# Performance work log

Measured on AMD Instinct MI355X. Metric: run time of the kernel, lower is better.

## Reference

```python
import jax, jax.numpy as jnp
import numpy as np

N = 40000      # nodes
E = 640000     # edges
D = 128        # embed_dim
H = 8          # heads
DH = D // H    # per-head dim
L = 3          # n_layers
IN = 64        # in_dim
FF = 218       # embed_dim2 (ffn hidden)
OUT = 1        # out_dim
EPS = 1e-5
NEG_SLOPE = 0.2


def setup_inputs() -> dict:
    key = jax.random.key(0)
    ks = jax.random.split(key, 16)
    nrm = lambda k, shape, s=0.1: (jax.random.normal(k, shape, jnp.float32) * s)
    return {
        "x": jax.random.normal(ks[0], (N, IN), jnp.float32),
        "src": jax.random.randint(ks[1], (E,), 0, N, jnp.int32),
        "dst": jax.random.randint(ks[2], (E,), 0, N, jnp.int32),
        "W_emb": nrm(ks[3], (IN, D)),
        "b_emb": jnp.zeros((D,), jnp.float32),
        "gat_W": nrm(ks[4], (L, D, D)),
        "attn_l": nrm(ks[5], (L, H, DH)),
        "attn_r": nrm(ks[6], (L, H, DH)),
        "gat_b": jnp.zeros((L, D), jnp.float32),
        "bn1_g": jnp.ones((L, D), jnp.float32),
        "bn1_b": jnp.zeros((L, D), jnp.float32),
        "ff_W1": nrm(ks[7], (L, D, FF)),
        "ff_b1": jnp.zeros((L, FF), jnp.float32),
        "ff_W2": nrm(ks[8], (L, FF, D)),
        "ff_b2": jnp.zeros((L, D), jnp.float32),
        "bn2_g": jnp.ones((L, D), jnp.float32),
        "bn2_b": jnp.zeros((L, D), jnp.float32),
        "dec_W1": nrm(ks[9], ((L + 1) * D, D)),
        "dec_bn_g": jnp.ones((D,), jnp.float32),
        "dec_bn_b": jnp.zeros((D,), jnp.float32),
        "dec_W2": nrm(ks[10], (D, OUT)),
    }


def _batchnorm(h, g, b):
    # BatchNorm1d in training mode: batch stats over nodes, biased variance
    mu = h.mean(axis=0)
    var = h.var(axis=0)
    return g * (h - mu) * jax.lax.rsqrt(var + EPS) + b


def _gat_layer(h, src, dst, W, al, ar, bias):
    n = h.shape[0]
    feat = (h @ W).reshape(n, H, DH)                      # [N,H,DH]
    el = (feat * al).sum(-1)                               # [N,H]
    er = (feat * ar).sum(-1)                               # [N,H]
    e = jax.nn.leaky_relu(el[src] + er[dst], NEG_SLOPE)    # [E,H]
    # segment softmax over incoming edges of each dst node
    emax = jax.ops.segment_max(e, dst, num_segments=n)
    ex = jnp.exp(e - emax[dst])
    den = jax.ops.segment_sum(ex, dst, num_segments=n)
    alpha = ex / den[dst]                                  # [E,H]
    msg = alpha[:, :, None] * feat[src]                    # [E,H,DH]
    out = jax.ops.segment_sum(msg, dst, num_segments=n)    # [N,H,DH]
    out = out + bias.reshape(H, DH)
    return out.reshape(n, D)


def reference(x, src, dst, W_emb, b_emb, gat_W, attn_l, attn_r, gat_b,
              bn1_g, bn1_b, ff_W1, ff_b1, ff_W2, ff_b2, bn2_g, bn2_b,
              dec_W1, dec_bn_g, dec_bn_b, dec_W2):
    h = x @ W_emb + b_emb                                  # embed_layer
    xs = [h]
    for l in range(L):
        # message passing with skip connection
        h = h + _gat_layer(h, src, dst, gat_W[l], attn_l[l], attn_r[l], gat_b[l])
        # feed forward: BN -> Skip(Linear,ReLU,Linear) -> BN
        h = _batchnorm(h, bn1_g[l], bn1_b[l])
        y = jax.nn.relu(h @ ff_W1[l] + ff_b1[l]) @ ff_W2[l] + ff_b2[l]
        h = _batchnorm(h + y, bn2_g[l], bn2_b[l])
        xs.append(h)
    h = jnp.concatenate(xs, axis=-1)                       # JumpingKnowledge 'cat'
    # decision MLP: relu(BN(h W1)) W2, no biases
    h = jax.nn.relu(_batchnorm(h @ dec_W1, dec_bn_g, dec_bn_b))
    return h @ dec_W2
```

## Files before the change

### kernel.cpp

```cpp
#include <hip/hip_runtime.h>
#include <hip/hip_bf16.h>
#include <math.h>

#define N_NODES 40000
#define N_EDGES 640000
#define DIM     128
#define HEADS   8
#define DHEAD   16
#define LAYERS  3
#define IN_DIM  64
#define FF_DIM  218
#define BN_EPS  1e-5f
#define NEG_SLOPE 0.2f
#define INV_N   (1.f / N_NODES)
#define NREP    128
#define AGG_NPW 2
#define AGG_BLOCKS (N_NODES / (4 * AGG_NPW))

typedef __attribute__((ext_vector_type(8))) short  bhalf8;
typedef __attribute__((ext_vector_type(4))) float  floatx4;
typedef __attribute__((ext_vector_type(4))) int    intx4;

__device__ __forceinline__ unsigned bfpack2(float a, float b) {
    unsigned ua = __float_as_uint(a);
    ua = ua + 0x7FFFu + ((ua >> 16) & 1u);
    unsigned ub = __float_as_uint(b);
    ub = ub + 0x7FFFu + ((ub >> 16) & 1u);
    return (ua >> 16) | (ub & 0xFFFF0000u);
}
__device__ __forceinline__ unsigned short bf16of(float a) {
    unsigned ua = __float_as_uint(a);
    ua = ua + 0x7FFFu + ((ua >> 16) & 1u);
    return (unsigned short)(ua >> 16);
}
__device__ __forceinline__ float bf2f(unsigned short u) {
    return __uint_as_float(((unsigned)u) << 16);
}
__device__ __forceinline__ float bflo(unsigned u) { return __uint_as_float(u << 16); }
__device__ __forceinline__ float bfhi(unsigned u) { return __uint_as_float(u & 0xFFFF0000u); }
__device__ __forceinline__ float rsum16(float v) {
    v += __shfl_xor(v, 1, 16);
    v += __shfl_xor(v, 2, 16);
    v += __shfl_xor(v, 4, 16);
    v += __shfl_xor(v, 8, 16);
    return v;
}

#define OFF_EMB 0
#define OFF_GAT 8192
#define OFF_W1  57344
#define OFF_W2  143360
#define OFF_DEC 229376
#define WPK_TOT 294912
#define HIST_BLOCKS ((N_EDGES + 255) / 256)
#define PACK_BLOCKS ((WPK_TOT + 255) / 256)

__global__ void hist_pack_kernel(const int* __restrict__ dst, int* __restrict__ counts,
                                 const float* __restrict__ W_emb,
                                 const float* __restrict__ gat_W,
                                 const float* __restrict__ ff_W1,
                                 const float* __restrict__ ff_W2,
                                 const float* __restrict__ dec_W1,
                                 unsigned short* __restrict__ wpk) {
    int bid = blockIdx.x;
    if (bid < HIST_BLOCKS) {
        int e = bid * 256 + threadIdx.x;
        if (e < N_EDGES) atomicAdd(&counts[dst[e]], 1);
        return;
    }
    int i = (bid - HIST_BLOCKS) * 256 + threadIdx.x;
    if (i >= WPK_TOT) return;
    int o = i;
    if (o < 8192) {
        int n = o >> 6, k = o & 63;
        wpk[OFF_EMB + o] = bf16of(W_emb[k * 128 + n]);
        return;
    }
    o -= 8192;
    if (o < 3 * 16384) {
        int l = o >> 14, r = o & 16383;
        int n = r >> 7, k = r & 127;
        wpk[OFF_GAT + o] = bf16of(gat_W[l * 16384 + k * 128 + n]);
        return;
    }
    o -= 3 * 16384;
    if (o < 3 * 28672) {
        int l = o / 28672, r = o % 28672;
        int n = r >> 7, k = r & 127;
        float v = (n < FF_DIM) ? ff_W1[(size_t)l * 128 * FF_DIM + k * FF_DIM + n] : 0.f;
        wpk[OFF_W1 + o] = bf16of(v);
        return;
    }
    o -= 3 * 28672;
    if (o < 3 * 28672) {
        int l = o / 28672, r = o % 28672;
        int n = r / 224, k = r % 224;
        float v = (k < FF_DIM) ? ff_W2[(size_t)l * FF_DIM * 128 + k * 128 + n] : 0.f;
        wpk[OFF_W2 + o] = bf16of(v);
        return;
    }
    o -= 3 * 28672;
    {
        int n = o >> 9, k = o & 511;
        wpk[OFF_DEC + o] = bf16of(dec_W1[k * 128 + n]);
    }
}

__global__ __launch_bounds__(1024) void scan_kernel(const int* __restrict__ counts,
                                                    int* __restrict__ indptr,
                                                    int* __restrict__ cursor, int n) {
    __shared__ int tsum[1024];
    const int CH = 40;
    int tid = threadIdx.x;
    int base = tid * CH;
    int loc[CH];
    int s = 0;
    #pragma unroll
    for (int i = 0; i < CH; i++) {
        int idx = base + i;
        int v = (idx < n) ? counts[idx] : 0;
        loc[i] = s;
        s += v;
    }
    tsum[tid] = s;
    __syncthreads();
    for (int offs = 1; offs < 1024; offs <<= 1) {
        int t = (tid >= offs) ? tsum[tid - offs] : 0;
        __syncthreads();
        tsum[tid] += t;
        __syncthreads();
    }
    int carry = (tid > 0) ? tsum[tid - 1] : 0;
    #pragma unroll
    for (int i = 0; i < CH; i++) {
        int idx = base + i;
        if (idx < n) {
            int v = carry + loc[i];
            indptr[idx] = v;
            cursor[idx] = v;
        }
    }
    if (tid == 1023) indptr[n] = tsum[1023];
}

__global__ void scatter_kernel(const int* __restrict__ src, const int* __restrict__ dst,
                               int* __restrict__ cursor,
                               int* __restrict__ srcs_csr) {
    int e = blockIdx.x * blockDim.x + threadIdx.x;
    if (e < N_EDGES) {
        int d = dst[e];
        int pos = atomicAdd(&cursor[d], 1);
        srcs_csr[pos] = src[e];
    }
}

template<int NT, int KPAD, int AMODE, bool ABF16, int MT, bool ELER, bool RESBF>
__global__ __launch_bounds__(256) void gemm_l2_kernel(
    const float* __restrict__ A, const unsigned short* __restrict__ Abf, int lda,
    const unsigned short* __restrict__ Bpk,
    const float* __restrict__ bias,
    const void* __restrict__ resv, int ldres,
    const float* __restrict__ res_stats, const float* __restrict__ res_g,
    const float* __restrict__ res_b,
    float* __restrict__ C, unsigned short* __restrict__ Cbf, int ldc,
    float* __restrict__ out_stats,
    int M, int Nact, int relu,
    const float* __restrict__ a_stats, float* __restrict__ a_stats_out,
    const float* __restrict__ a_g, const float* __restrict__ a_b,
    const float* __restrict__ al, const float* __restrict__ ar,
    float* __restrict__ el_out, float* __restrict__ er_out)
{
    constexpr int SCN = (AMODE > 0) ? KPAD : 1;
    constexpr int BROWS = 64 * MT;
    constexpr int STEPS = KPAD / 32;
    constexpr int CST = (STEPS > 2) ? 2 : STEPS;
    __shared__ float sc_s[SCN];
    __shared__ float sh_s[SCN];
    __shared__ float st_sum[128];
    __shared__ float st_sq[128];
    __shared__ float el_s[ELER ? BROWS : 1][ELER ? NT : 1];
    __shared__ float er_s[ELER ? BROWS : 1][ELER ? NT : 1];

    int tid = threadIdx.x, wave = tid >> 6, lane = tid & 63;
    int q = lane >> 4, tl = lane & 15;
    int colbase = blockIdx.y * (NT * 16);
    int row0b = blockIdx.x * BROWS;
    int rowtile = row0b + wave * (MT * 16);

    if constexpr (AMODE == 1 || AMODE == 2) {
        for (int idx = tid; idx < KPAD; idx += 256) {
            float scv = 1.f, shv = 0.f;
            if constexpr (AMODE == 1) {
                float mu = a_stats[idx] * INV_N;
                float var = a_stats[128 + idx] * INV_N - mu * mu;
                scv = a_g[idx] * rsqrtf(var + BN_EPS);
                shv = a_b[idx] - mu * scv;
            } else {
                int l = idx >> 7;
                if (l > 0) {
                    int c = idx & 127;
                    const float* st = a_stats + (l - 1) * 256;
                    float mu = st[c] * INV_N;
                    float var = st[128 + c] * INV_N - mu * mu;
                    scv = a_g[(l - 1) * 128 + c] * rsqrtf(var + BN_EPS);
                    shv = a_b[(l - 1) * 128 + c] - mu * scv;
                }
            }
            sc_s[idx] = scv;
            sh_s[idx] = shv;
        }
        __syncthreads();
    }
    if constexpr (AMODE == 3) {
        for (int idx = tid; idx < 128; idx += 256) {
            float s = 0.f, sq = 0.f;
            #pragma unroll 8
            for (int r = 0; r < NREP; r++) {
                s  += a_stats[r * 256 + idx];
                sq += a_stats[r * 256 + 128 + idx];
            }
            a_stats_out[idx] = s;
            a_stats_out[128 + idx] = sq;
            float mu = s * INV_N;
            float var = sq * INV_N - mu * mu;
            float scv = a_g[idx] * rsqrtf(var + BN_EPS);
            sc_s[idx] = scv;
            sh_s[idx] = a_b[idx] - mu * scv;
        }
        __syncthreads();
    }

    int rowm[MT];
    bool vrm[MT];
    #pragma unroll
    for (int mt = 0; mt < MT; mt++) {
        rowm[mt] = rowtile + mt * 16 + tl;
        vrm[mt] = rowm[mt] < M;
    }
    const unsigned short* bp = Bpk + (size_t)colbase * KPAD;

    floatx4 acc[MT][NT] = {};

    #pragma unroll
    for (int c0 = 0; c0 < STEPS; c0 += CST) {
        intx4  arawb[CST][MT];
        floatx4 araw0[ABF16 ? 1 : CST][ABF16 ? 1 : MT];
        floatx4 araw1[ABF16 ? 1 : CST][ABF16 ? 1 : MT];
        bhalf8 breg[CST][NT];
        #pragma unroll
        for (int cs = 0; cs < CST; cs++) {
            if (c0 + cs >= STEPS) continue;
            int gk = (c0 + cs) * 32 + q * 8;
            #pragma unroll
            for (int j = 0; j < NT; j++)
                breg[cs][j] = *(const bhalf8*)(bp + (size_t)(j * 16 + tl) * KPAD + gk);
            #pragma unroll
            for (int mt = 0; mt < MT; mt++) {
                if constexpr (ABF16) {
                    intx4 u = {};
                    if (vrm[mt]) u = *(const intx4*)(Abf + (size_t)rowm[mt] * lda + gk);
                    arawb[cs][mt] = u;
                } else {
                    floatx4 x0 = {}, x1 = {};
                    if (vrm[mt]) {
                        const float* ap = A + (size_t)rowm[mt] * lda + gk;
                        x0 = *(const floatx4*)ap;
                        x1 = *(const floatx4*)(ap + 4);
                    }
                    araw0[cs][mt] = x0;
                    araw1[cs][mt] = x1;
                }
            }
        }
        #pragma unroll
        for (int cs = 0; cs < CST; cs++) {
            if (c0 + cs >= STEPS) continue;
            int gk = (c0 + cs) * 32 + q * 8;
            bhalf8 af[MT];
            #pragma unroll
            for (int mt = 0; mt < MT; mt++) {
                if constexpr (ABF16) {
                    intx4 u = arawb[cs][mt];
                    if constexpr (AMODE > 0) {
                        #pragma unroll
                        for (int w = 0; w < 4; w++) {
                            unsigned uw = (unsigned)u[w];
                            float lo = bflo(uw), hi = bfhi(uw);
                            lo = fmaf(sc_s[gk + 2 * w],     lo, sh_s[gk + 2 * w]);
                            hi = fmaf(sc_s[gk + 2 * w + 1], hi, sh_s[gk + 2 * w + 1]);
                            u[w] = (int)bfpack2(lo, hi);
                        }
                    }
                    af[mt] = *(bhalf8*)&u;
                } else {
                    floatx4 x0 = araw0[cs][mt], x1 = araw1[cs][mt];
                    if constexpr (AMODE > 0) {
                        #pragma unroll
                        for (int jj = 0; jj < 4; jj++) {
                            x0[jj] = fmaf(sc_s[gk + jj],     x0[jj], sh_s[gk + jj]);
                            x1[jj] = fmaf(sc_s[gk + 4 + jj], x1[jj], sh_s[gk + 4 + jj]);
                        }
                    }
                    intx4 t = intx4{(int)bfpack2(x0[0], x0[1]), (int)bfpack2(x0[2], x0[3]),
                                    (int)bfpack2(x1[0], x1[1]), (int)bfpack2(x1[2], x1[3])};
                    af[mt] = *(bhalf8*)&t;
                }
            }
            #pragma unroll
            for (int mt = 0; mt < MT; mt++)
                #pragma unroll
                for (int j = 0; j < NT; j++)
                    acc[mt][j] = __builtin_amdgcn_mfma_f32_16x16x32_bf16(af[mt], breg[cs][j], acc[mt][j], 0, 0, 0);
        }
    }

    float psum[NT], psq[NT];
    #pragma unroll
    for (int j = 0; j < NT; j++) { psum[j] = 0.f; psq[j] = 0.f; }

    #pragma unroll
    for (int j = 0; j < NT; j++) {
        int c = colbase + j * 16 + tl;
        bool cok = c < Nact;
        float bv = (bias && cok) ? bias[c] : 0.f;
        float rsc = 1.f, rsh = 0.f;
        if (res_stats && cok) {
            float mu = res_stats[c] * INV_N;
            float var = res_stats[128 + c] * INV_N - mu * mu;
            rsc = res_g[c] * rsqrtf(var + BN_EPS);
            rsh = res_b[c] - mu * rsc;
        }
        float alc = 0.f, arc = 0.f;
        if constexpr (ELER) { alc = al[c]; arc = ar[c]; }
        #pragma unroll
        for (int mt = 0; mt < MT; mt++) {
            #pragma unroll
            for (int reg = 0; reg < 4; reg++) {
                int r = rowtile + mt * 16 + q * 4 + reg;
                bool rok = r < M;
                float v = 0.f;
                if (rok && cok) {
                    v = acc[mt][j][reg] + bv;
                    if (resv) {
                        size_t ri = (size_t)r * ldres + c;
                        float rv = RESBF ? bf2f(((const unsigned short*)resv)[ri])
                                         : ((const float*)resv)[ri];
                        v = fmaf(rsc, rv, v + rsh);
                    }
                    if (relu) v = fmaxf(v, 0.f);
                    if (out_stats) { psum[j] += v; psq[j] = fmaf(v, v, psq[j]); }
                }
                if constexpr (ELER) {
                    float pel = rsum16(v * alc);
                    float per_ = rsum16(v * arc);
                    if (tl == 0) {
                        int rl = wave * (MT * 16) + mt * 16 + q * 4 + reg;
                        el_s[rl][j] = pel;
                        er_s[rl][j] = per_;
                    }
                }
                if (rok) {
                    if (Cbf) Cbf[(size_t)r * ldc + c] = bf16of(v);
                    else if (cok) C[(size_t)r * ldc + c] = v;
                }
            }
        }
    }

    if constexpr (ELER) {
        __syncthreads();
        int gh = blockIdx.y * NT;
        for (int idx = tid; idx < BROWS * NT; idx += 256) {
            int rl = idx / NT, hj = idx % NT;
            int r = row0b + rl;
            if (r < M) {
                el_out[(size_t)r * 8 + gh + hj] = el_s[rl][hj];
                er_out[(size_t)r * 8 + gh + hj] = er_s[rl][hj];
            }
        }
    }

    if (out_stats) {
        __syncthreads();
        if (tid < 128) { st_sum[tid] = 0.f; st_sq[tid] = 0.f; }
        __syncthreads();
        #pragma unroll
        for (int j = 0; j < NT; j++) {
            int c = colbase + j * 16 + tl;
            if (c < 128) { atomicAdd(&st_sum[c], psum[j]); atomicAdd(&st_sq[c], psq[j]); }
        }
        __syncthreads();
        if (tid < 128) {
            atomicAdd(&out_stats[tid], st_sum[tid]);
            atomicAdd(&out_stats[128 + tid], st_sq[tid]);
        }
    }
}

__global__ __launch_bounds__(256) void gat_aggregate_kernel(
    const unsigned short* __restrict__ feat,
    const float* __restrict__ el, const float* __restrict__ er,
    const int* __restrict__ indptr, const int* __restrict__ srcs_csr,
    const unsigned short* __restrict__ h_in, int ldh,
    const float* __restrict__ hstats, const float* __restrict__ hg,
    const float* __restrict__ hb,
    const float* __restrict__ bias,
    unsigned short* __restrict__ outp,
    float* __restrict__ stats_rep)
{
    int t = threadIdx.x;
    int w = t >> 6, lane = t & 63;
    int d0 = lane * 2;
    int hh = lane >> 3;
    int pick = lane & 3;
    int gb = lane & 56;
    __shared__ float sred[4][128];
    __shared__ float qred[4][128];

    float aff_s0 = 1.f, aff_h0 = 0.f, aff_s1 = 1.f, aff_h1 = 0.f;
    if (hstats) {
        float mu0 = hstats[d0] * INV_N;
        float v0  = hstats[128 + d0] * INV_N - mu0 * mu0;
        aff_s0 = hg[d0] * rsqrtf(v0 + BN_EPS);
        aff_h0 = hb[d0] - mu0 * aff_s0;
        float mu1 = hstats[d0 + 1] * INV_N;
        float v1  = hstats[128 + d0 + 1] * INV_N - mu1 * mu1;
        aff_s1 = hg[d0 + 1] * rsqrtf(v1 + BN_EPS);
        aff_h1 = hb[d0 + 1] - mu1 * aff_s1;
    }
    float b0 = bias[d0], b1 = bias[d0 + 1];

    float ss0 = 0.f, sq0 = 0.f, ss1 = 0.f, sq1 = 0.f;
    int nbase = (blockIdx.x * 4 + w) * AGG_NPW;
    #pragma unroll
    for (int ni = 0; ni < AGG_NPW; ni++) {
        int n = nbase + ni;
        if (n >= N_NODES) break;
        int beg = indptr[n], end = indptr[n + 1];
        float ern = er[(size_t)n * 8 + hh];
        float acc0 = 0.f, acc1 = 0.f, den = 0.f;
        int i = beg;
        for (; i + 3 < end; i += 4) {
            int s0 = srcs_csr[i],     s1 = srcs_csr[i + 1];
            int s2 = srcs_csr[i + 2], s3 = srcs_csr[i + 3];
            int sp = pick == 0 ? s0 : pick == 1 ? s1 : pick == 2 ? s2 : s3;
            float ee = el[(size_t)sp * 8 + hh] + ern;
            unsigned f0 = *(const unsigned*)(feat + (size_t)s0 * DIM + d0);
            unsigned f1 = *(const unsigned*)(feat + (size_t)s1 * DIM + d0);
            unsigned f2 = *(const unsigned*)(feat + (size_t)s2 * DIM + d0);
            unsigned f3 = *(const unsigned*)(feat + (size_t)s3 * DIM + d0);
            float aa = expf(ee > 0.f ? ee : NEG_SLOPE * ee);
            float a0 = __shfl(aa, gb + 0);
            float a1 = __shfl(aa, gb + 1);
            float a2 = __shfl(aa, gb + 2);
            float a3 = __shfl(aa, gb + 3);
            den += (a0 + a1) + (a2 + a3);
            acc0 = fmaf(a0, bflo(f0), acc0); acc1 = fmaf(a0, bfhi(f0), acc1);
            acc0 = fmaf(a1, bflo(f1), acc0); acc1 = fmaf(a1, bfhi(f1), acc1);
            acc0 = fmaf(a2, bflo(f2), acc0); acc1 = fmaf(a2, bfhi(f2), acc1);
            acc0 = fmaf(a3, bflo(f3), acc0); acc1 = fmaf(a3, bfhi(f3), acc1);
        }
        for (; i < end; i++) {
            int s0 = srcs_csr[i];
            float e0 = el[(size_t)s0 * 8 + hh] + ern;
            unsigned f0 = *(const unsigned*)(feat + (size_t)s0 * DIM + d0);
            float a0 = expf(e0 > 0.f ? e0 : NEG_SLOPE * e0);
            den += a0;
            acc0 = fmaf(a0, bflo(f0), acc0);
            acc1 = fmaf(a0, bfhi(f0), acc1);
        }
        float inv = den > 0.f ? 1.f / den : 0.f;
        unsigned hu = *(const unsigned*)(h_in + (size_t)n * ldh + d0);
        float hv0 = fmaf(aff_s0, bflo(hu), aff_h0);
        float hv1 = fmaf(aff_s1, bfhi(hu), aff_h1);
        unsigned short u0 = bf16of(hv0 + acc0 * inv + b0);
        unsigned short u1 = bf16of(hv1 + acc1 * inv + b1);
        *(unsigned*)(outp + (size_t)n * DIM + d0) = ((unsigned)u0) | (((unsigned)u1) << 16);
        float vr0 = bf2f(u0), vr1 = bf2f(u1);
        ss0 += vr0; sq0 = fmaf(vr0, vr0, sq0);
        ss1 += vr1; sq1 = fmaf(vr1, vr1, sq1);
    }
    sred[w][d0] = ss0; sred[w][d0 + 1] = ss1;
    qred[w][d0] = sq0; qred[w][d0 + 1] = sq1;
    __syncthreads();
    {
        int d = t & 127;
        float v = (t < 128)
            ? (sred[0][d] + sred[1][d]) + (sred[2][d] + sred[3][d])
            : (qred[0][d] + qred[1][d]) + (qred[2][d] + qred[3][d]);
        float* rep = stats_rep + ((size_t)(blockIdx.x & (NREP - 1)) << 8);
        atomicAdd(&rep[t], v);
    }
}

__global__ __launch_bounds__(256) void decide_kernel(
    const unsigned short* __restrict__ z, const float* __restrict__ stats,
    const float* __restrict__ g, const float* __restrict__ b,
    const float* __restrict__ W2, float* __restrict__ outp, int M)
{
    int wid = threadIdx.x >> 6, lane = threadIdx.x & 63;
    int n = blockIdx.x * 4 + wid;
    if (n >= M) return;
    float acc = 0.f;
    #pragma unroll
    for (int cc = 0; cc < 2; cc++) {
        int c = lane + cc * 64;
        float mu  = stats[c] * INV_N;
        float var = stats[DIM + c] * INV_N - mu * mu;
        float v = fmaf(g[c] * rsqrtf(var + BN_EPS), bf2f(z[(size_t)n * DIM + c]) - mu, b[c]);
        v = fmaxf(v, 0.f);
        acc = fmaf(v, W2[c], acc);
    }
    #pragma unroll
    for (int offs = 32; offs > 0; offs >>= 1)
        acc += __shfl_down(acc, offs);
    if (lane == 0) outp[n] = acc;
}

extern "C" void kernel_launch(void* const* d_in, const int* in_sizes, int n_in,
                              void* d_out, int out_size, void* d_ws, size_t ws_size,
                              hipStream_t stream)
{
    const float* x      = (const float*)d_in[0];
    const int*   src    = (const int*)  d_in[1];
    const int*   dst    = (const int*)  d_in[2];
    const float* W_emb  = (const float*)d_in[3];
    const float* b_emb  = (const float*)d_in[4];
    const float* gat_W  = (const float*)d_in[5];
    const float* attn_l = (const float*)d_in[6];
    const float* attn_r = (const float*)d_in[7];
    const float* gat_b  = (const float*)d_in[8];
    const float* bn1_g  = (const float*)d_in[9];
    const float* bn1_b  = (const float*)d_in[10];
    const float* ff_W1  = (const float*)d_in[11];
    const float* ff_b1  = (const float*)d_in[12];
    const float* ff_W2  = (const float*)d_in[13];
    const float* ff_b2  = (const float*)d_in[14];
    const float* bn2_g  = (const float*)d_in[15];
    const float* bn2_b  = (const float*)d_in[16];
    const float* dec_W1 = (const float*)d_in[17];
    const float* dec_bn_g = (const float*)d_in[18];
    const float* dec_bn_b = (const float*)d_in[19];
    const float* dec_W2 = (const float*)d_in[20];
    float* outp = (float*)d_out;

    char* ws = (char*)d_ws;
    size_t off = 0;
    auto alloc = [&](size_t bytes) -> void* {
        void* p = ws + off;
        off += (bytes + 255) & ~(size_t)255;
        return p;
    };
    unsigned short* xsb = (unsigned short*)alloc((size_t)N_NODES * 512 * 2);
    unsigned short* zb  = (unsigned short*)alloc((size_t)N_NODES * DIM * 2);
    unsigned short* featb = (unsigned short*)alloc((size_t)N_NODES * DIM * 2);
    float* el    = (float*)alloc((size_t)N_NODES * HEADS * 4);
    float* er    = (float*)alloc((size_t)N_NODES * HEADS * 4);
    unsigned short* y1b = (unsigned short*)alloc((size_t)N_NODES * 224 * 2);
    unsigned short* btb = (unsigned short*)alloc((size_t)N_NODES * DIM * 2);
    int*   counts= (int*)  alloc((size_t)N_NODES * 4);
    float* statsAll = (float*)alloc(((size_t)3 * NREP * 256 + 7 * 256) * 4);
    unsigned short* wpk = (unsigned short*)alloc((size_t)WPK_TOT * 2);
    int*   indptr= (int*)  alloc((size_t)(N_NODES + 1) * 4);
    int*   cursor= (int*)  alloc((size_t)N_NODES * 4);
    int*   srcs_csr = (int*)alloc((size_t)N_EDGES * 4);
    (void)ws_size; (void)in_sizes; (void)n_in; (void)out_size;

    float* rep1   = statsAll;
    float* stats1c= statsAll + 3 * NREP * 256;
    float* stats2 = statsAll + 3 * NREP * 256 + 3 * 256;
    float* statsD = statsAll + 3 * NREP * 256 + 6 * 256;

    dim3 gg2((N_NODES + 127) / 128, 2);
    dim3 ggdec((N_NODES + 63) / 64, 2);

    hipMemsetAsync(counts, 0, (size_t)N_NODES * 4 + ((size_t)3 * NREP * 256 + 7 * 256) * 4, stream);
    hist_pack_kernel<<<HIST_BLOCKS + PACK_BLOCKS, 256, 0, stream>>>(
        dst, counts, W_emb, gat_W, ff_W1, ff_W2, dec_W1, wpk);
    scan_kernel<<<1, 1024, 0, stream>>>(counts, indptr, cursor, N_NODES);
    scatter_kernel<<<(N_EDGES + 255) / 256, 256, 0, stream>>>(src, dst, cursor, srcs_csr);

    gemm_l2_kernel<4, 64, 0, false, 2, false, false><<<gg2, 256, 0, stream>>>(
        x, nullptr, IN_DIM, wpk + OFF_EMB, b_emb,
        nullptr, 0, nullptr, nullptr, nullptr,
        nullptr, xsb, 512, nullptr,
        N_NODES, DIM, 0, nullptr, nullptr, nullptr, nullptr,
        nullptr, nullptr, nullptr, nullptr);

    for (int l = 0; l < LAYERS; l++) {
        const unsigned short* h_cur = xsb + (size_t)l * DIM;
        const float* hstats = l ? stats2 + (l - 1) * 256 : nullptr;
        const float* hg = l ? bn2_g + (l - 1) * DIM : nullptr;
        const float* hb = l ? bn2_b + (l - 1) * DIM : nullptr;
        if (l == 0)
            gemm_l2_kernel<4, 128, 0, true, 2, true, false><<<gg2, 256, 0, stream>>>(
                nullptr, h_cur, 512, wpk + OFF_GAT + l * 16384, nullptr,
                nullptr, 0, nullptr, nullptr, nullptr,
                nullptr, featb, DIM, nullptr,
                N_NODES, DIM, 0, nullptr, nullptr, nullptr, nullptr,
                attn_l + l * DIM, attn_r + l * DIM, el, er);
        else
            gemm_l2_kernel<4, 128, 1, true, 2, true, false><<<gg2, 256, 0, stream>>>(
                nullptr, h_cur, 512, wpk + OFF_GAT + l * 16384, nullptr,
                nullptr, 0, nullptr, nullptr, nullptr,
                nullptr, featb, DIM, nullptr,
                N_NODES, DIM, 0, hstats, nullptr, hg, hb,
                attn_l + l * DIM, attn_r + l * DIM, el, er);
        gat_aggregate_kernel<<<AGG_BLOCKS, 256, 0, stream>>>(
            featb, el, er, indptr, srcs_csr, h_cur, 512,
            hstats, hg, hb, gat_b + l * DIM, btb,
            rep1 + (size_t)l * NREP * 256);
        gemm_l2_kernel<7, 128, 3, true, 2, false, false><<<gg2, 256, 0, stream>>>(
            nullptr, btb, DIM, wpk + OFF_W1 + l * 28672,
            ff_b1 + l * FF_DIM,
            nullptr, 0, nullptr, nullptr, nullptr,
            nullptr, y1b, 224, nullptr,
            N_NODES, FF_DIM, 1,
            rep1 + (size_t)l * NREP * 256, stats1c + l * 256,
            bn1_g + l * DIM, bn1_b + l * DIM,
            nullptr, nullptr, nullptr, nullptr);
        gemm_l2_kernel<4, 224, 0, true, 2, false, true><<<gg2, 256, 0, stream>>>(
            nullptr, y1b, 224, wpk + OFF_W2 + l * 28672,
            ff_b2 + l * DIM,
            btb, DIM, stats1c + l * 256, bn1_g + l * DIM, bn1_b + l * DIM,
            nullptr, xsb + (size_t)(l + 1) * DIM, 512, stats2 + l * 256,
            N_NODES, DIM, 0, nullptr, nullptr, nullptr, nullptr,
            nullptr, nullptr, nullptr, nullptr);
    }

    gemm_l2_kernel<4, 512, 2, true, 1, false, false><<<ggdec, 256, 0, stream>>>(
        nullptr, xsb, 512, wpk + OFF_DEC, nullptr,
        nullptr, 0, nullptr, nullptr, nullptr,
        nullptr, zb, DIM, statsD,
        N_NODES, DIM, 0, stats2, nullptr, bn2_g, bn2_b,
        nullptr, nullptr, nullptr, nullptr);
    decide_kernel<<<(N_NODES + 3) / 4, 256, 0, stream>>>(
        zb, statsD, dec_bn_g, dec_bn_b, dec_W2, outp, N_NODES);
}
```

Measured before the change: 716.3 us.

## Stage A tiles in swizzled shared memory for bf16 GEMM kernels

Adds a STAGEA template path where each block cooperatively loads a chunk of up to 128 K-columns of the bf16 A rows into LDS with an XOR swizzle, then waves read their A fragments from LDS. Global A loads become coalesced row-contiguous 16-byte accesses instead of per-lane strided fragment gathers. In exchange it adds shared memory use (up to 32 KB per block at MT=2), __syncthreads barriers, and loses the previous register prefetch overlap of A and B loads. All bf16-input GEMMs switch to this path; the fp32 embedding GEMM keeps the old one.

```diff
diff --git a/kernel.cpp b/kernel.cpp
--- a/kernel.cpp
+++ b/kernel.cpp
@@ -154,7 +154,7 @@
     }
 }
 
-template<int NT, int KPAD, int AMODE, bool ABF16, int MT, bool ELER, bool RESBF>
+template<int NT, int KPAD, int AMODE, bool ABF16, int MT, bool ELER, bool RESBF, bool STAGEA>
 __global__ __launch_bounds__(256) void gemm_l2_kernel(
     const float* __restrict__ A, const unsigned short* __restrict__ Abf, int lda,
     const unsigned short* __restrict__ Bpk,
@@ -180,6 +180,7 @@
     __shared__ float st_sq[128];
     __shared__ float el_s[ELER ? BROWS : 1][ELER ? NT : 1];
     __shared__ float er_s[ELER ? BROWS : 1][ELER ? NT : 1];
+    __shared__ unsigned short As[STAGEA ? BROWS * 128 : 1];
 
     int tid = threadIdx.x, wave = tid >> 6, lane = tid & 63;
     int q = lane >> 4, tl = lane & 15;
@@ -230,57 +231,37 @@
         __syncthreads();
     }
 
-    int rowm[MT];
-    bool vrm[MT];
-    #pragma unroll
-    for (int mt = 0; mt < MT; mt++) {
-        rowm[mt] = rowtile + mt * 16 + tl;
-        vrm[mt] = rowm[mt] < M;
-    }
     const unsigned short* bp = Bpk + (size_t)colbase * KPAD;
 
     floatx4 acc[MT][NT] = {};
 
-    #pragma unroll
-    for (int c0 = 0; c0 < STEPS; c0 += CST) {
-        intx4  arawb[CST][MT];
-        floatx4 araw0[ABF16 ? 1 : CST][ABF16 ? 1 : MT];
-        floatx4 araw1[ABF16 ? 1 : CST][ABF16 ? 1 : MT];
-        bhalf8 breg[CST][NT];
+    if constexpr (STAGEA) {
+        char* asb = (char*)As;
         #pragma unroll
-        for (int cs = 0; cs < CST; cs++) {
-            if (c0 + cs >= STEPS) continue;
-            int gk = (c0 + cs) * 32 + q * 8;
+        for (int ck = 0; ck < STEPS; ck += 4) {
+            int csteps = (STEPS - ck) < 4 ? (STEPS - ck) : 4;
+            int ck16 = csteps * 4;
+            for (int idx = tid; idx < BROWS * ck16; idx += 256) {
+                int lr = idx / ck16, kc = idx - lr * ck16;
+                int rg = row0b + lr;
+                intx4 u = {};
+                if (rg < M) u = *(const intx4*)(Abf + (size_t)rg * lda + ck * 32 + kc * 8);
+                *(intx4*)(asb + lr * 256 + ((kc ^ (lr & 7)) << 4)) = u;
+            }
+            __syncthreads();
             #pragma unroll
-            for (int j = 0; j < NT; j++)
-                breg[cs][j] = *(const bhalf8*)(bp + (size_t)(j * 16 + tl) * KPAD + gk);
-            #pragma unroll
-            for (int mt = 0; mt < MT; mt++) {
-                if constexpr (ABF16) {
-                    intx4 u = {};
-                    if (vrm[mt]) u = *(const intx4*)(Abf + (size_t)rowm[mt] * lda + gk);
-                    arawb[cs][mt] = u;
-                } else {
-                    floatx4 x0 = {}, x1 = {};
-                    if (vrm[mt]) {
-                        const float* ap = A + (size_t)rowm[mt] * lda + gk;
-                        x0 = *(const floatx4*)ap;
-                        x1 = *(const floatx4*)(ap + 4);
-                    }
-                    araw0[cs][mt] = x0;
-                    araw1[cs][mt] = x1;
-                }
-            }
-        }
-        #pragma unroll
-        for (int cs = 0; cs < CST; cs++) {
-            if (c0 + cs >= STEPS) continue;
-            int gk = (c0 + cs) * 32 + q * 8;
-            bhalf8 af[MT];
-            #pragma unroll
-            for (int mt = 0; mt < MT; mt++) {
-                if constexpr (ABF16) {
-                    intx4 u = arawb[cs][mt];
+            for (int cs = 0; cs < 4; cs++) {
+                if (cs >= csteps) break;
+                int gk = (ck + cs) * 32 + q * 8;
+                bhalf8 breg2[NT];
+                #pragma unroll
+                for (int j = 0; j < NT; j++)
+                    breg2[j] = *(const bhalf8*)(bp + (size_t)(j * 16 + tl) * KPAD + gk);
+                bhalf8 af[MT];
+                #pragma unroll
+                for (int mt = 0; mt < MT; mt++) {
+                    int lr = wave * (MT * 16) + mt * 16 + tl;
+                    intx4 u = *(const intx4*)(asb + lr * 256 + (((cs * 4 + q) ^ (lr & 7)) << 4));
                     if constexpr (AMODE > 0) {
                         #pragma unroll
                         for (int w = 0; w < 4; w++) {
@@ -292,25 +273,94 @@
                         }
                     }
                     af[mt] = *(bhalf8*)&u;
-                } else {
-                    floatx4 x0 = araw0[cs][mt], x1 = araw1[cs][mt];
-                    if constexpr (AMODE > 0) {
-                        #pragma unroll
-                        for (int jj = 0; jj < 4; jj++) {
-                            x0[jj] = fmaf(sc_s[gk + jj],     x0[jj], sh_s[gk + jj]);
-                            x1[jj] = fmaf(sc_s[gk + 4 + jj], x1[jj], sh_s[gk + 4 + jj]);
-                        }
-                    }
-                    intx4 t = intx4{(int)bfpack2(x0[0], x0[1]), (int)bfpack2(x0[2], x0[3]),
-                                    (int)bfpack2(x1[0], x1[1]), (int)bfpack2(x1[2], x1[3])};
-                    af[mt] = *(bhalf8*)&t;
                 }
-            }
+                #pragma unroll
+                for (int mt = 0; mt < MT; mt++)
+                    #pragma unroll
+                    for (int j = 0; j < NT; j++)
+                        acc[mt][j] = __builtin_amdgcn_mfma_f32_16x16x32_bf16(af[mt], breg2[j], acc[mt][j], 0, 0, 0);
+            }
+            __syncthreads();
+        }
+    } else {
+        int rowm[MT];
+        bool vrm[MT];
+        #pragma unroll
+        for (int mt = 0; mt < MT; mt++) {
+            rowm[mt] = rowtile + mt * 16 + tl;
+            vrm[mt] = rowm[mt] < M;
+        }
+        #pragma unroll
+        for (int c0 = 0; c0 < STEPS; c0 += CST) {
+            intx4  arawb[CST][MT];
+            floatx4 araw0[ABF16 ? 1 : CST][ABF16 ? 1 : MT];
+            floatx4 araw1[ABF16 ? 1 : CST][ABF16 ? 1 : MT];
+            bhalf8 breg[CST][NT];
             #pragma unroll
-            for (int mt = 0; mt < MT; mt++)
+            for (int cs = 0; cs < CST; cs++) {
+                if (c0 + cs >= STEPS) continue;
+                int gk = (c0 + cs) * 32 + q * 8;
                 #pragma unroll
                 for (int j = 0; j < NT; j++)
-                    acc[mt][j] = __builtin_amdgcn_mfma_f32_16x16x32_bf16(af[mt], breg[cs][j], acc[mt][j], 0, 0, 0);
+                    breg[cs][j] = *(const bhalf8*)(bp + (size_t)(j * 16 + tl) * KPAD + gk);
+                #pragma unroll
+                for (int mt = 0; mt < MT; mt++) {
+                    if constexpr (ABF16) {
+                        intx4 u = {};
+                        if (vrm[mt]) u = *(const intx4*)(Abf + (size_t)rowm[mt] * lda + gk);
+                        arawb[cs][mt] = u;
+                    } else {
+                        floatx4 x0 = {}, x1 = {};
+                        if (vrm[mt]) {
+                            const float* ap = A + (size_t)rowm[mt] * lda + gk;
+                            x0 = *(const floatx4*)ap;
+                            x1 = *(const floatx4*)(ap + 4);
+                        }
+                        araw0[cs][mt] = x0;
+                        araw1[cs][mt] = x1;
+                    }
+                }
+            }
+            #pragma unroll
+            for (int cs = 0; cs < CST; cs++) {
+                if (c0 + cs >= STEPS) continue;
+                int gk = (c0 + cs) * 32 + q * 8;
+                bhalf8 af[MT];
+                #pragma unroll
+                for (int mt = 0; mt < MT; mt++) {
+                    if constexpr (ABF16) {
+                        intx4 u = arawb[cs][mt];
+                        if constexpr (AMODE > 0) {
+                            #pragma unroll
+                            for (int w = 0; w < 4; w++) {
+                                unsigned uw = (unsigned)u[w];
+                                float lo = bflo(uw), hi = bfhi(uw);
+                                lo = fmaf(sc_s[gk + 2 * w],     lo, sh_s[gk + 2 * w]);
+                                hi = fmaf(sc_s[gk + 2 * w + 1], hi, sh_s[gk + 2 * w + 1]);
+                                u[w] = (int)bfpack2(lo, hi);
+                            }
+                        }
+                        af[mt] = *(bhalf8*)&u;
+                    } else {
+                        floatx4 x0 = araw0[cs][mt], x1 = araw1[cs][mt];
+                        if constexpr (AMODE > 0) {
+                            #pragma unroll
+                            for (int jj = 0; jj < 4; jj++) {
+                                x0[jj] = fmaf(sc_s[gk + jj],     x0[jj], sh_s[gk + jj]);
+                                x1[jj] = fmaf(sc_s[gk + 4 + jj], x1[jj], sh_s[gk + 4 + jj]);
+                            }
+                        }
+                        intx4 t = intx4{(int)bfpack2(x0[0], x0[1]), (int)bfpack2(x0[2], x0[3]),
+                                        (int)bfpack2(x1[0], x1[1]), (int)bfpack2(x1[2], x1[3])};
+                        af[mt] = *(bhalf8*)&t;
+                    }
+                }
+                #pragma unroll
+                for (int mt = 0; mt < MT; mt++)
+                    #pragma unroll
+                    for (int j = 0; j < NT; j++)
+                        acc[mt][j] = __builtin_amdgcn_mfma_f32_16x16x32_bf16(af[mt], breg[cs][j], acc[mt][j], 0, 0, 0);
+            }
         }
     }
 
@@ -580,7 +630,7 @@
     scan_kernel<<<1, 1024, 0, stream>>>(counts, indptr, cursor, N_NODES);
     scatter_kernel<<<(N_EDGES + 255) / 256, 256, 0, stream>>>(src, dst, cursor, srcs_csr);
 
-    gemm_l2_kernel<4, 64, 0, false, 2, false, false><<<gg2, 256, 0, stream>>>(
+    gemm_l2_kernel<4, 64, 0, false, 2, false, false, false><<<gg2, 256, 0, stream>>>(
         x, nullptr, IN_DIM, wpk + OFF_EMB, b_emb,
         nullptr, 0, nullptr, nullptr, nullptr,
         nullptr, xsb, 512, nullptr,
@@ -593,14 +643,14 @@
         const float* hg = l ? bn2_g + (l - 1) * DIM : nullptr;
         const float* hb = l ? bn2_b + (l - 1) * DIM : nullptr;
         if (l == 0)
-            gemm_l2_kernel<4, 128, 0, true, 2, true, false><<<gg2, 256, 0, stream>>>(
+            gemm_l2_kernel<4, 128, 0, true, 2, true, false, true><<<gg2, 256, 0, stream>>>(
                 nullptr, h_cur, 512, wpk + OFF_GAT + l * 16384, nullptr,
                 nullptr, 0, nullptr, nullptr, nullptr,
                 nullptr, featb, DIM, nullptr,
                 N_NODES, DIM, 0, nullptr, nullptr, nullptr, nullptr,
                 attn_l + l * DIM, attn_r + l * DIM, el, er);
         else
-            gemm_l2_kernel<4, 128, 1, true, 2, true, false><<<gg2, 256, 0, stream>>>(
+            gemm_l2_kernel<4, 128, 1, true, 2, true, false, true><<<gg2, 256, 0, stream>>>(
                 nullptr, h_cur, 512, wpk + OFF_GAT + l * 16384, nullptr,
                 nullptr, 0, nullptr, nullptr, nullptr,
                 nullptr, featb, DIM, nullptr,
@@ -610,7 +660,7 @@
             featb, el, er, indptr, srcs_csr, h_cur, 512,
             hstats, hg, hb, gat_b + l * DIM, btb,
             rep1 + (size_t)l * NREP * 256);
-        gemm_l2_kernel<7, 128, 3, true, 2, false, false><<<gg2, 256, 0, stream>>>(
+        gemm_l2_kernel<7, 128, 3, true, 2, false, false, true><<<gg2, 256, 0, stream>>>(
             nullptr, btb, DIM, wpk + OFF_W1 + l * 28672,
             ff_b1 + l * FF_DIM,
             nullptr, 0, nullptr, nullptr, nullptr,
@@ -619,7 +669,7 @@
             rep1 + (size_t)l * NREP * 256, stats1c + l * 256,
             bn1_g + l * DIM, bn1_b + l * DIM,
             nullptr, nullptr, nullptr, nullptr);
-        gemm_l2_kernel<4, 224, 0, true, 2, false, true><<<gg2, 256, 0, stream>>>(
+        gemm_l2_kernel<4, 224, 0, true, 2, false, true, true><<<gg2, 256, 0, stream>>>(
             nullptr, y1b, 224, wpk + OFF_W2 + l * 28672,
             ff_b2 + l * DIM,
             btb, DIM, stats1c + l * 256, bn1_g + l * DIM, bn1_b + l * DIM,
@@ -628,7 +678,7 @@
             nullptr, nullptr, nullptr, nullptr);
     }
 
-    gemm_l2_kernel<4, 512, 2, true, 1, false, false><<<ggdec, 256, 0, stream>>>(
+    gemm_l2_kernel<4, 512, 2, true, 1, false, false, true><<<ggdec, 256, 0, stream>>>(
         nullptr, xsb, 512, wpk + OFF_DEC, nullptr,
         nullptr, 0, nullptr, nullptr, nullptr,
         nullptr, zb, DIM, statsD,
```

Measured after the change: 742.3 us. 1.04x slower.

## Stage GEMM weights in LDS and software-pipeline bf16 A-tile loads

Applied to the files above, without the earlier changes.

For bf16-input GEMMs, each block now copies its weight column slice into padded shared memory once, and the K loop reads B from LDS rather than global memory. A-row loads are prefetched several K-steps ahead in a rotating register buffer. The decoder GEMM also switches to narrower column tiles (NT 4→2) over twice as many column blocks. The goal is to hide global-load latency and cut redundant weight reads, at the cost of more LDS use (the 512-wide decoder stages about 33 KB) and higher register pressure, which could lower occupancy.

```diff
diff --git a/kernel.cpp b/kernel.cpp
--- a/kernel.cpp
+++ b/kernel.cpp
@@ -173,19 +173,30 @@
     constexpr int SCN = (AMODE > 0) ? KPAD : 1;
     constexpr int BROWS = 64 * MT;
     constexpr int STEPS = KPAD / 32;
-    constexpr int CST = (STEPS > 2) ? 2 : STEPS;
+    constexpr int BPK = KPAD + 8;
     __shared__ float sc_s[SCN];
     __shared__ float sh_s[SCN];
     __shared__ float st_sum[128];
     __shared__ float st_sq[128];
     __shared__ float el_s[ELER ? BROWS : 1][ELER ? NT : 1];
     __shared__ float er_s[ELER ? BROWS : 1][ELER ? NT : 1];
+    __shared__ unsigned short Bs[ABF16 ? NT * 16 * BPK : 1];
 
     int tid = threadIdx.x, wave = tid >> 6, lane = tid & 63;
     int q = lane >> 4, tl = lane & 15;
     int colbase = blockIdx.y * (NT * 16);
     int row0b = blockIdx.x * BROWS;
     int rowtile = row0b + wave * (MT * 16);
+
+    const unsigned short* bp = Bpk + (size_t)colbase * KPAD;
+
+    if constexpr (ABF16) {
+        for (int idx = tid; idx < NT * 16 * (KPAD / 8); idx += 256) {
+            int col = idx / (KPAD / 8), k8 = idx % (KPAD / 8);
+            *(intx4*)(Bs + col * BPK + k8 * 8) =
+                *(const intx4*)(bp + (size_t)col * KPAD + k8 * 8);
+        }
+    }
 
     if constexpr (AMODE == 1 || AMODE == 2) {
         for (int idx = tid; idx < KPAD; idx += 256) {
@@ -209,7 +220,6 @@
             sc_s[idx] = scv;
             sh_s[idx] = shv;
         }
-        __syncthreads();
     }
     if constexpr (AMODE == 3) {
         for (int idx = tid; idx < 128; idx += 256) {
@@ -227,8 +237,8 @@
             sc_s[idx] = scv;
             sh_s[idx] = a_b[idx] - mu * scv;
         }
-        __syncthreads();
-    }
+    }
+    if constexpr (ABF16 || AMODE > 0) __syncthreads();
 
     int rowm[MT];
     bool vrm[MT];
@@ -237,80 +247,103 @@
         rowm[mt] = rowtile + mt * 16 + tl;
         vrm[mt] = rowm[mt] < M;
     }
-    const unsigned short* bp = Bpk + (size_t)colbase * KPAD;
 
     floatx4 acc[MT][NT] = {};
 
-    #pragma unroll
-    for (int c0 = 0; c0 < STEPS; c0 += CST) {
-        intx4  arawb[CST][MT];
-        floatx4 araw0[ABF16 ? 1 : CST][ABF16 ? 1 : MT];
-        floatx4 araw1[ABF16 ? 1 : CST][ABF16 ? 1 : MT];
-        bhalf8 breg[CST][NT];
+    if constexpr (ABF16) {
+        constexpr int PD = (STEPS >= 4) ? 4 : STEPS;
+        intx4 ap[PD][MT];
         #pragma unroll
-        for (int cs = 0; cs < CST; cs++) {
-            if (c0 + cs >= STEPS) continue;
-            int gk = (c0 + cs) * 32 + q * 8;
+        for (int s = 0; s < PD - 1; s++) {
+            int gk = s * 32 + q * 8;
+            #pragma unroll
+            for (int mt = 0; mt < MT; mt++) {
+                intx4 u = {};
+                if (vrm[mt]) u = *(const intx4*)(Abf + (size_t)rowm[mt] * lda + gk);
+                ap[s][mt] = u;
+            }
+        }
+        #pragma unroll
+        for (int s = 0; s < STEPS; s++) {
+            int gk = s * 32 + q * 8;
+            if (s + PD - 1 < STEPS) {
+                int gk2 = (s + PD - 1) * 32 + q * 8;
+                #pragma unroll
+                for (int mt = 0; mt < MT; mt++) {
+                    intx4 u = {};
+                    if (vrm[mt]) u = *(const intx4*)(Abf + (size_t)rowm[mt] * lda + gk2);
+                    ap[(s + PD - 1) % PD][mt] = u;
+                }
+            }
+            bhalf8 breg[NT];
             #pragma unroll
             for (int j = 0; j < NT; j++)
-                breg[cs][j] = *(const bhalf8*)(bp + (size_t)(j * 16 + tl) * KPAD + gk);
-            #pragma unroll
-            for (int mt = 0; mt < MT; mt++) {
-                if constexpr (ABF16) {
-                    intx4 u = {};
-                    if (vrm[mt]) u = *(const intx4*)(Abf + (size_t)rowm[mt] * lda + gk);
-                    arawb[cs][mt] = u;
-                } else {
-                    floatx4 x0 = {}, x1 = {};
-                    if (vrm[mt]) {
-                        const float* ap = A + (size_t)rowm[mt] * lda + gk;
-                        x0 = *(const floatx4*)ap;
-                        x1 = *(const floatx4*)(ap + 4);
-                    }
-                    araw0[cs][mt] = x0;
-                    araw1[cs][mt] = x1;
-                }
-            }
-        }
-        #pragma unroll
-        for (int cs = 0; cs < CST; cs++) {
-            if (c0 + cs >= STEPS) continue;
-            int gk = (c0 + cs) * 32 + q * 8;
+                breg[j] = *(const bhalf8*)(Bs + (j * 16 + tl) * BPK + gk);
             bhalf8 af[MT];
             #pragma unroll
             for (int mt = 0; mt < MT; mt++) {
-                if constexpr (ABF16) {
-                    intx4 u = arawb[cs][mt];
-                    if constexpr (AMODE > 0) {
-                        #pragma unroll
-                        for (int w = 0; w < 4; w++) {
-                            unsigned uw = (unsigned)u[w];
-                            float lo = bflo(uw), hi = bfhi(uw);
-                            lo = fmaf(sc_s[gk + 2 * w],     lo, sh_s[gk + 2 * w]);
-                            hi = fmaf(sc_s[gk + 2 * w + 1], hi, sh_s[gk + 2 * w + 1]);
-                            u[w] = (int)bfpack2(lo, hi);
-                        }
+                intx4 u = ap[s % PD][mt];
+                if constexpr (AMODE > 0) {
+                    #pragma unroll
+                    for (int w = 0; w < 4; w++) {
+                        unsigned uw = (unsigned)u[w];
+                        float lo = bflo(uw), hi = bfhi(uw);
+                        lo = fmaf(sc_s[gk + 2 * w],     lo, sh_s[gk + 2 * w]);
+                        hi = fmaf(sc_s[gk + 2 * w + 1], hi, sh_s[gk + 2 * w + 1]);
+                        u[w] = (int)bfpack2(lo, hi);
                     }
-                    af[mt] = *(bhalf8*)&u;
-                } else {
-                    floatx4 x0 = araw0[cs][mt], x1 = araw1[cs][mt];
-                    if constexpr (AMODE > 0) {
-                        #pragma unroll
-                        for (int jj = 0; jj < 4; jj++) {
-                            x0[jj] = fmaf(sc_s[gk + jj],     x0[jj], sh_s[gk + jj]);
-                            x1[jj] = fmaf(sc_s[gk + 4 + jj], x1[jj], sh_s[gk + 4 + jj]);
-                        }
-                    }
-                    intx4 t = intx4{(int)bfpack2(x0[0], x0[1]), (int)bfpack2(x0[2], x0[3]),
-                                    (int)bfpack2(x1[0], x1[1]), (int)bfpack2(x1[2], x1[3])};
-                    af[mt] = *(bhalf8*)&t;
-                }
+                }
+                af[mt] = *(bhalf8*)&u;
             }
             #pragma unroll
             for (int mt = 0; mt < MT; mt++)
                 #pragma unroll
                 for (int j = 0; j < NT; j++)
-                    acc[mt][j] = __builtin_amdgcn_mfma_f32_16x16x32_bf16(af[mt], breg[cs][j], acc[mt][j], 0, 0, 0);
+                    acc[mt][j] = __builtin_amdgcn_mfma_f32_16x16x32_bf16(af[mt], breg[j], acc[mt][j], 0, 0, 0);
+        }
+    } else {
+        constexpr int CST = (STEPS > 2) ? 2 : STEPS;
+        #pragma unroll
+        for (int c0 = 0; c0 < STEPS; c0 += CST) {
+            floatx4 araw0[CST][MT];
+            floatx4 araw1[CST][MT];
+            bhalf8 breg[CST][NT];
+            #pragma unroll
+            for (int cs = 0; cs < CST; cs++) {
+                if (c0 + cs >= STEPS) continue;
+                int gk = (c0 + cs) * 32 + q * 8;
+                #pragma unroll
+                for (int j = 0; j < NT; j++)
+                    breg[cs][j] = *(const bhalf8*)(bp + (size_t)(j * 16 + tl) * KPAD + gk);
+                #pragma unroll
+                for (int mt = 0; mt < MT; mt++) {
+                    floatx4 x0 = {}, x1 = {};
+                    if (vrm[mt]) {
+                        const float* apt = A + (size_t)rowm[mt] * lda + gk;
+                        x0 = *(const floatx4*)apt;
+                        x1 = *(const floatx4*)(apt + 4);
+                    }
+                    araw0[cs][mt] = x0;
+                    araw1[cs][mt] = x1;
+                }
+            }
+            #pragma unroll
+            for (int cs = 0; cs < CST; cs++) {
+                if (c0 + cs >= STEPS) continue;
+                bhalf8 af[MT];
+                #pragma unroll
+                for (int mt = 0; mt < MT; mt++) {
+                    floatx4 x0 = araw0[cs][mt], x1 = araw1[cs][mt];
+                    intx4 t = intx4{(int)bfpack2(x0[0], x0[1]), (int)bfpack2(x0[2], x0[3]),
+                                    (int)bfpack2(x1[0], x1[1]), (int)bfpack2(x1[2], x1[3])};
+                    af[mt] = *(bhalf8*)&t;
+                }
+                #pragma unroll
+                for (int mt = 0; mt < MT; mt++)
+                    #pragma unroll
+                    for (int j = 0; j < NT; j++)
+                        acc[mt][j] = __builtin_amdgcn_mfma_f32_16x16x32_bf16(af[mt], breg[cs][j], acc[mt][j], 0, 0, 0);
+            }
         }
     }
 
@@ -572,7 +605,7 @@
     float* statsD = statsAll + 3 * NREP * 256 + 6 * 256;
 
     dim3 gg2((N_NODES + 127) / 128, 2);
-    dim3 ggdec((N_NODES + 63) / 64, 2);
+    dim3 ggdec((N_NODES + 63) / 64, 4);
 
     hipMemsetAsync(counts, 0, (size_t)N_NODES * 4 + ((size_t)3 * NREP * 256 + 7 * 256) * 4, stream);
     hist_pack_kernel<<<HIST_BLOCKS + PACK_BLOCKS, 256, 0, stream>>>(
@@ -628,7 +661,7 @@
             nullptr, nullptr, nullptr, nullptr);
     }
 
-    gemm_l2_kernel<4, 512, 2, true, 1, false, false><<<ggdec, 256, 0, stream>>>(
+    gemm_l2_kernel<2, 512, 2, true, 1, false, false><<<ggdec, 256, 0, stream>>>(
         nullptr, xsb, 512, wpk + OFF_DEC, nullptr,
         nullptr, 0, nullptr, nullptr, nullptr,
         nullptr, zb, DIM, statsD,
```

Result: slower. 762.1 us (+6.4%).
